# Kernel optimization log

Hardware: AMD Instinct MI355X
Metric: run time of the kernel (lower is better)

Reference implementation:

```python
import jax, jax.numpy as jnp
import numpy as np

EPS = 1e-12  # F.normalize default eps (denominator = max(norm, eps))


def setup_inputs() -> dict:
    key = jax.random.key(0)
    ks = jax.random.split(key, 8)
    B, FIN, H, W = 4, 256, 64, 64
    N_MEM, SQ = 64, 16           # sqrt_fin = fin**0.5
    POS_CH = 2                    # PosEncoding concatenates one coord channel per dim
    CIN = FIN + POS_CH
    QK = N_MEM * SQ               # 1024
    # PosEncoding buffer: normalized coordinate grid in [-1, 1], shape [2, H, W]
    ys = jnp.linspace(-1.0, 1.0, H, dtype=jnp.float32)
    xs = jnp.linspace(-1.0, 1.0, W, dtype=jnp.float32)
    gy, gx = jnp.meshgrid(ys, xs, indexing='ij')
    pos = jnp.stack([gy, gx], axis=0)
    s = 0.02
    return {
        'x':    jax.random.normal(ks[0], (B, FIN, H, W), jnp.float32),
        'pos':  pos,
        'wq':   jax.random.normal(ks[1], (QK, CIN), jnp.float32) * s,
        'bq':   jnp.zeros((QK,), jnp.float32),
        'wk':   jax.random.normal(ks[2], (QK, CIN), jnp.float32) * s,
        'bk':   jnp.zeros((QK,), jnp.float32),
        'v':    jax.random.normal(ks[3], (N_MEM, FIN), jnp.float32) * s,
        'wout': jax.random.normal(ks[4], (FIN, FIN), jnp.float32) * s,
        'bout': jnp.zeros((FIN,), jnp.float32),
    }


def reference(x, pos, wq, bq, wk, bk, v, wout, bout):
    B, C, H, W = x.shape
    S = H * W
    n_mem, fin = v.shape
    sq = wq.shape[0] // n_mem
    # PosEncoding: concat coordinate channels
    posb = jnp.broadcast_to(pos[None], (B,) + pos.shape)
    xp = jnp.concatenate([x, posb], axis=1).reshape(B, C + pos.shape[0], S)
    # 1x1 conv projections (channel GEMMs)
    q = jnp.einsum('oc,bcs->bos', wq, xp) + bq[None, :, None]  # [B, n_mem*sq, S]
    k = jnp.einsum('oc,bcs->bos', wk, xp) + bk[None, :, None]
    q = q.reshape(B, n_mem, sq, S).transpose(0, 3, 1, 2)  # [B,S,m,sq]
    k = k.reshape(B, n_mem, sq, S).transpose(0, 3, 2, 1)  # [B,S,sq,m]
    # F.normalize: q over last dim (sqrt_fin), k over dim=1 (sqrt_fin)
    qn = q / jnp.maximum(jnp.linalg.norm(q, axis=-1, keepdims=True), EPS)
    kn = k / jnp.maximum(jnp.linalg.norm(k, axis=2, keepdims=True), EPS)
    # attn[b,s,m,n] = qn . kn ; dropout is identity in eval mode.
    # mean over memory slots m commutes with (attn @ v), so fuse:
    attn_mean = jnp.einsum('bsk,bskn->bsn', qn.mean(axis=2), kn)  # [B,S,n_mem]
    mem = attn_mean @ v                                            # [B,S,fin]
    mem = mem.transpose(0, 2, 1).reshape(B, fin, H, W)
    out = jnp.einsum('of,bfhw->bohw', wout, mem) + bout[None, :, None, None]
    return x + out
```

## Files before the change

kernel.cpp:

```cpp
#include <hip/hip_runtime.h>
#include <stdint.h>

#define EPSN 1e-12f

typedef float f32x16 __attribute__((ext_vector_type(16)));
typedef float f32x4 __attribute__((ext_vector_type(4)));
typedef __bf16 bf16x8 __attribute__((ext_vector_type(8)));
typedef uint32_t u32x4 __attribute__((ext_vector_type(4)));

__device__ __forceinline__ unsigned short f2bf(float f) {
  union { float f; unsigned int u; } v; v.f = f;
  unsigned int u = v.u + 0x7FFFu + ((v.u >> 16) & 1u);
  return (unsigned short)(u >> 16);
}

__device__ __forceinline__ void dma16(const void* g, void* l) {
  __builtin_amdgcn_global_load_lds(
      (const __attribute__((address_space(1))) unsigned int*)g,
      (__attribute__((address_space(3))) unsigned int*)l, 16, 0, 0);
}

#define WQF_OFF 0
#define WKF_OFF (32 * 18 * 64 * 8)
#define WVP_OFF (2 * 32 * 18 * 64 * 8)

__global__ __launch_bounds__(256) void prep_kernel(
    const float* __restrict__ wq, const float* __restrict__ bq,
    const float* __restrict__ wk, const float* __restrict__ bk,
    const float* __restrict__ v, const float* __restrict__ wout,
    unsigned short* __restrict__ wsp) {
  if (blockIdx.x < 288) {
    int t2 = blockIdx.x * 256 + threadIdx.x;
    int isK = t2 >= 36864;
    int t = isK ? t2 - 36864 : t2;
    const float* w = isK ? wk : wq;
    const float* bb = isK ? bk : bq;
    unsigned short* dst = wsp + (isK ? WKF_OFF : WQF_OFF);
    int lane = t & 63, rest = t >> 6;
    int ks = rest % 18, g = rest / 18;
    int o = g * 32 + (lane & 31);
    int kb = ks * 16 + (lane >> 5) * 8;
    unsigned short v8[8];
#pragma unroll
    for (int j = 0; j < 8; ++j) {
      int k = kb + j;
      float val;
      if (k < 258)       val = w[o * 258 + k];
      else if (k == 258) val = bb[o];
      else               val = 0.f;
      v8[j] = f2bf(val);
    }
    *(u32x4*)(dst + t * 8) = *(u32x4*)v8;
  } else {
    int idx2 = (blockIdx.x - 288) * 256 + threadIdx.x;
    int fc = idx2 & 3, m = (idx2 >> 2) & 63, o = idx2 >> 8;
    const f32x4* wo = (const f32x4*)(wout + o * 256 + fc * 64);
    const f32x4* vm = (const f32x4*)(v + m * 256 + fc * 64);
    float s = 0.f;
#pragma unroll
    for (int f = 0; f < 16; ++f) {
      f32x4 a = wo[f], bvv = vm[f];
      s += a[0]*bvv[0] + a[1]*bvv[1] + a[2]*bvv[2] + a[3]*bvv[3];
    }
    s += __shfl_xor(s, 1, 64);
    s += __shfl_xor(s, 2, 64);
    if (fc == 0) wsp[WVP_OFF + o * 64 + m] = f2bf(s);
  }
}

#define KP 296
#define QS 66
#define AT 72

__global__ __launch_bounds__(1024, 4) void fused_kernel(
    const float* __restrict__ x, const float* __restrict__ pos,
    const unsigned short* __restrict__ wsp, const float* __restrict__ bout,
    float* __restrict__ out) {
  __shared__ __align__(16) unsigned short aBuf[3 * 32 * 512];
  __shared__ __align__(16) unsigned short xp[64 * KP];
  __shared__ __align__(16) float qbarL[16 * QS];
  __shared__ __align__(16) unsigned short attnM[64 * AT];
  __shared__ float boutL[256];

  const int tid = threadIdx.x;
  const int lane = tid & 63;
  const int wid = __builtin_amdgcn_readfirstlane(tid >> 6);
  const int px = lane & 31, q2 = lane >> 5;
  const int P0 = blockIdx.x * 64;
  const int b = P0 >> 12, s0 = P0 & 4095;

  uint32_t* xp32 = (uint32_t*)xp;
  for (int i = tid; i < 64 * 152; i += 1024) {
    int dc = i & 7, pp = (i >> 3) & 63, dh = i >> 9;
    int dcol = dh * 8 + dc;
    if (dcol < 148) {
      int c0 = dcol * 2;
      float v0, v1;
      if (c0 < 256) {
        v0 = x[(b * 256 + c0) * 4096 + s0 + pp];
        v1 = x[(b * 256 + c0 + 1) * 4096 + s0 + pp];
      } else if (c0 == 256) {
        v0 = pos[s0 + pp];
        v1 = pos[4096 + s0 + pp];
      } else {
        v0 = (c0 == 258) ? 1.0f : 0.0f;
        v1 = 0.0f;
      }
      xp32[pp * 148 + dcol] = (uint32_t)f2bf(v0) | ((uint32_t)f2bf(v1) << 16);
    }
  }
  if (tid < 256) boutL[tid] = bout[tid];
  for (int i = tid; i < 16 * QS; i += 1024) qbarL[i] = 0.f;
  __syncthreads();

#define ISSUE(wb, ks_) do {                                              \
    int _sl = (ks_) % 3;                                                 \
    dma16(wb + ((2 * wid) * 18 + (ks_)) * 512 + lane * 8,                \
          &aBuf[_sl * 16384 + (2 * wid) * 512]);                         \
    dma16(wb + ((2 * wid + 1) * 18 + (ks_)) * 512 + lane * 8,            \
          &aBuf[_sl * 16384 + (2 * wid + 1) * 512]);                     \
  } while (0)

#define COMPUTE(ks_) do {                                                \
    int _sl = (ks_) % 3;                                                 \
    bf16x8 _a0 = *(const bf16x8*)&aBuf[_sl * 16384 + (2 * wid) * 512 + lane * 8];     \
    bf16x8 _a1 = *(const bf16x8*)&aBuf[_sl * 16384 + (2 * wid + 1) * 512 + lane * 8]; \
    bf16x8 _b0 = *(const bf16x8*)&xp[px * KP + (ks_) * 16 + q2 * 8];     \
    bf16x8 _b1 = *(const bf16x8*)&xp[(32 + px) * KP + (ks_) * 16 + q2 * 8]; \
    acc00 = __builtin_amdgcn_mfma_f32_32x32x16_bf16(_a0, _b0, acc00, 0, 0, 0); \
    acc01 = __builtin_amdgcn_mfma_f32_32x32x16_bf16(_a0, _b1, acc01, 0, 0, 0); \
    acc10 = __builtin_amdgcn_mfma_f32_32x32x16_bf16(_a1, _b0, acc10, 0, 0, 0); \
    acc11 = __builtin_amdgcn_mfma_f32_32x32x16_bf16(_a1, _b1, acc11, 0, 0, 0); \
  } while (0)

#define PHASE(wb) do {                                                   \
    ISSUE(wb, 0); ISSUE(wb, 1);                                          \
    _Pragma("unroll 4")                                                  \
    for (int ks = 0; ks < 16; ++ks) {                                    \
      asm volatile("" ::: "memory");                                     \
      ISSUE(wb, ks + 2);                                                 \
      asm volatile("s_waitcnt vmcnt(4)" ::: "memory");                   \
      COMPUTE(ks);                                                       \
    }                                                                    \
    asm volatile("s_waitcnt vmcnt(2)" ::: "memory");                     \
    COMPUTE(16);                                                         \
    asm volatile("s_waitcnt vmcnt(0)" ::: "memory");                     \
    COMPUTE(17);                                                         \
  } while (0)

  f32x16 acc00 = (f32x16)0.f, acc01 = (f32x16)0.f,
         acc10 = (f32x16)0.f, acc11 = (f32x16)0.f;
  PHASE((wsp + WQF_OFF));

  {
    float qsum[2][8];
#pragma unroll
    for (int nt = 0; nt < 2; ++nt)
#pragma unroll
      for (int r = 0; r < 8; ++r) qsum[nt][r] = 0.f;
#pragma unroll
    for (int ot = 0; ot < 2; ++ot) {
#pragma unroll
      for (int nt = 0; nt < 2; ++nt) {
        const f32x16 a = ot ? (nt ? acc11 : acc10) : (nt ? acc01 : acc00);
        float s20 = 0.f, s21 = 0.f;
#pragma unroll
        for (int r = 0; r < 8; ++r) {
          s20 = fmaf(a[r], a[r], s20);
          s21 = fmaf(a[r + 8], a[r + 8], s21);
        }
        s20 += __shfl_xor(s20, 32, 64);
        s21 += __shfl_xor(s21, 32, 64);
        float i0 = 1.0f / fmaxf(sqrtf(s20), EPSN);
        float i1 = 1.0f / fmaxf(sqrtf(s21), EPSN);
#pragma unroll
        for (int r = 0; r < 8; ++r) qsum[nt][r] += a[r] * i0 + a[r + 8] * i1;
      }
    }
#pragma unroll
    for (int nt = 0; nt < 2; ++nt)
#pragma unroll
      for (int r = 0; r < 8; ++r) {
        int j = (r & 3) + ((r >> 2) << 3) + (q2 << 2);
        atomicAdd(&qbarL[j * QS + nt * 32 + px], qsum[nt][r] * (1.0f / 64.0f));
      }
  }
  __syncthreads();

  acc00 = (f32x16)0.f; acc01 = (f32x16)0.f;
  acc10 = (f32x16)0.f; acc11 = (f32x16)0.f;
  PHASE((wsp + WKF_OFF));

  {
    float qb[2][8];
#pragma unroll
    for (int nt = 0; nt < 2; ++nt)
#pragma unroll
      for (int r = 0; r < 8; ++r) {
        int j = (r & 3) + ((r >> 2) << 3) + (q2 << 2);
        qb[nt][r] = qbarL[j * QS + nt * 32 + px];
      }
#pragma unroll
    for (int ot = 0; ot < 2; ++ot) {
#pragma unroll
      for (int nt = 0; nt < 2; ++nt) {
        const f32x16 a = ot ? (nt ? acc11 : acc10) : (nt ? acc01 : acc00);
        float s20 = 0.f, s21 = 0.f, sp0 = 0.f, sp1 = 0.f;
#pragma unroll
        for (int r = 0; r < 8; ++r) {
          s20 = fmaf(a[r], a[r], s20);         sp0 = fmaf(qb[nt][r], a[r], sp0);
          s21 = fmaf(a[r + 8], a[r + 8], s21); sp1 = fmaf(qb[nt][r], a[r + 8], sp1);
        }
        s20 += __shfl_xor(s20, 32, 64);
        s21 += __shfl_xor(s21, 32, 64);
        sp0 += __shfl_xor(sp0, 32, 64);
        sp1 += __shfl_xor(sp1, 32, 64);
        if (q2 == 0) {
          int m0 = wid * 4 + ot * 2;
          attnM[(nt * 32 + px) * AT + m0]     = f2bf(sp0 / fmaxf(sqrtf(s20), EPSN));
          attnM[(nt * 32 + px) * AT + m0 + 1] = f2bf(sp1 / fmaxf(sqrtf(s21), EPSN));
        }
      }
    }
  }
  __syncthreads();

  {
    const int otile = wid >> 1, pxt = wid & 1;
    f32x16 e = (f32x16)0.f;
    const unsigned short* wv = wsp + WVP_OFF + (otile * 32 + px) * 64 + q2 * 8;
    const unsigned short* ab = &attnM[(pxt * 32 + px) * AT + q2 * 8];
#pragma unroll
    for (int ks = 0; ks < 4; ++ks) {
      bf16x8 av = *(const bf16x8*)(wv + ks * 16);
      bf16x8 bv = *(const bf16x8*)(ab + ks * 16);
      e = __builtin_amdgcn_mfma_f32_32x32x16_bf16(av, bv, e, 0, 0, 0);
    }
#pragma unroll
    for (int r = 0; r < 16; ++r) {
      const int o = otile * 32 + (r & 3) + ((r >> 2) << 3) + (q2 << 2);
      const int p = pxt * 32 + px;
      const int gi = (b * 256 + o) * 4096 + s0 + p;
      out[gi] = x[gi] + boutL[o] + e[r];
    }
  }
#undef PHASE
#undef COMPUTE
#undef ISSUE
}

extern "C" void kernel_launch(void* const* d_in, const int* in_sizes, int n_in,
                              void* d_out, int out_size, void* d_ws, size_t ws_size,
                              hipStream_t stream) {
  const float* x    = (const float*)d_in[0];
  const float* pos  = (const float*)d_in[1];
  const float* wq   = (const float*)d_in[2];
  const float* bq   = (const float*)d_in[3];
  const float* wk   = (const float*)d_in[4];
  const float* bk   = (const float*)d_in[5];
  const float* v    = (const float*)d_in[6];
  const float* wout = (const float*)d_in[7];
  const float* bout = (const float*)d_in[8];
  float* out = (float*)d_out;
  unsigned short* wsp = (unsigned short*)d_ws;

  hipLaunchKernelGGL(prep_kernel, dim3(544), dim3(256), 0, stream,
                     wq, bq, wk, bk, v, wout, wsp);
  hipLaunchKernelGGL(fused_kernel, dim3(256), dim3(1024), 0, stream,
                     x, pos, wsp, bout, out);
}
```

Baseline: 136.3 us.

## Coalesce weight prep reads, widen wout·v reduction, prefetch A tiles earlier

The prep kernel now reads wq/wk rows contiguously as float2 and scatters them into the MFMA fragment layout. Previously each thread gathered eight strided values. The wout·v fold is split across 16 lanes instead of 4, which launches more blocks. In the fused kernel, the first two DMA weight stages are issued before the x staging loop, and the K-phase prefetch is issued before the Q normalization epilogue, so global latency overlaps other work. B-operand LDS loads are also hoisted ahead of the DMA issue. The early K prefetch relies on the omitted middle section no longer issuing its own initial stages, which raises a risk of slot conflicts with aBuf.

```diff
diff --git a/kernel.cpp b/kernel.cpp
--- a/kernel.cpp
+++ b/kernel.cpp
@@ -6,7 +6,6 @@
 typedef float f32x16 __attribute__((ext_vector_type(16)));
 typedef float f32x4 __attribute__((ext_vector_type(4)));
 typedef __bf16 bf16x8 __attribute__((ext_vector_type(8)));
-typedef uint32_t u32x4 __attribute__((ext_vector_type(4)));
 
 __device__ __forceinline__ unsigned short f2bf(float f) {
   union { float f; unsigned int u; } v; v.f = f;
@@ -29,41 +28,45 @@
     const float* __restrict__ wk, const float* __restrict__ bk,
     const float* __restrict__ v, const float* __restrict__ wout,
     unsigned short* __restrict__ wsp) {
-  if (blockIdx.x < 288) {
-    int t2 = blockIdx.x * 256 + threadIdx.x;
-    int isK = t2 >= 36864;
-    int t = isK ? t2 - 36864 : t2;
+  int bid = blockIdx.x;
+  if (bid < 512) {
+    int isK = bid >= 256;
+    int ob = (bid & 255) * 4;
     const float* w = isK ? wk : wq;
     const float* bb = isK ? bk : bq;
     unsigned short* dst = wsp + (isK ? WKF_OFF : WQF_OFF);
-    int lane = t & 63, rest = t >> 6;
-    int ks = rest % 18, g = rest / 18;
-    int o = g * 32 + (lane & 31);
-    int kb = ks * 16 + (lane >> 5) * 8;
-    unsigned short v8[8];
-#pragma unroll
-    for (int j = 0; j < 8; ++j) {
-      int k = kb + j;
-      float val;
-      if (k < 258)       val = w[o * 258 + k];
-      else if (k == 258) val = bb[o];
-      else               val = 0.f;
-      v8[j] = f2bf(val);
-    }
-    *(u32x4*)(dst + t * 8) = *(u32x4*)v8;
+    for (int i = threadIdx.x; i < 4 * 129; i += 256) {
+      int r = i / 129, q = i - r * 129;
+      int o = ob + r, k = q * 2;
+      float2 w2 = *(const float2*)(w + o * 258 + k);
+      int g = o >> 5, col = o & 31;
+      int ks = k >> 4, hi = (k >> 3) & 1, j = k & 7;
+      uint32_t pk = (uint32_t)f2bf(w2.x) | ((uint32_t)f2bf(w2.y) << 16);
+      *(uint32_t*)(dst + (((g * 18 + ks) * 64 + hi * 32 + col) << 3) + j) = pk;
+    }
+    for (int i = threadIdx.x; i < 4 * 30; i += 256) {
+      int r = i / 30, kk = 258 + (i - r * 30);
+      int o = ob + r;
+      int g = o >> 5, col = o & 31;
+      int ks = kk >> 4, hi = (kk >> 3) & 1, j = kk & 7;
+      dst[(((g * 18 + ks) * 64 + hi * 32 + col) << 3) + j] =
+          (kk == 258) ? f2bf(bb[o]) : (unsigned short)0;
+    }
   } else {
-    int idx2 = (blockIdx.x - 288) * 256 + threadIdx.x;
-    int fc = idx2 & 3, m = (idx2 >> 2) & 63, o = idx2 >> 8;
-    const f32x4* wo = (const f32x4*)(wout + o * 256 + fc * 64);
-    const f32x4* vm = (const f32x4*)(v + m * 256 + fc * 64);
+    int idx = (bid - 512) * 256 + threadIdx.x;
+    int fc = idx & 15, m = (idx >> 4) & 63, o = idx >> 10;
+    const f32x4* wo = (const f32x4*)(wout + o * 256 + fc * 16);
+    const f32x4* vm = (const f32x4*)(v + m * 256 + fc * 16);
     float s = 0.f;
 #pragma unroll
-    for (int f = 0; f < 16; ++f) {
+    for (int f = 0; f < 4; ++f) {
       f32x4 a = wo[f], bvv = vm[f];
       s += a[0]*bvv[0] + a[1]*bvv[1] + a[2]*bvv[2] + a[3]*bvv[3];
     }
     s += __shfl_xor(s, 1, 64);
     s += __shfl_xor(s, 2, 64);
+    s += __shfl_xor(s, 4, 64);
+    s += __shfl_xor(s, 8, 64);
     if (fc == 0) wsp[WVP_OFF + o * 64 + m] = f2bf(s);
   }
 }
@@ -88,6 +91,17 @@
   const int px = lane & 31, q2 = lane >> 5;
   const int P0 = blockIdx.x * 64;
   const int b = P0 >> 12, s0 = P0 & 4095;
+
+#define ISSUE(wb, ks_) do {                                              \
+    int _sl = (ks_) % 3;                                                 \
+    dma16(wb + ((2 * wid) * 18 + (ks_)) * 512 + lane * 8,                \
+          &aBuf[_sl * 16384 + (2 * wid) * 512]);                         \
+    dma16(wb + ((2 * wid + 1) * 18 + (ks_)) * 512 + lane * 8,            \
+          &aBuf[_sl * 16384 + (2 * wid + 1) * 512]);                     \
+  } while (0)
+
+  ISSUE((wsp + WQF_OFF), 0);
+  ISSUE((wsp + WQF_OFF), 1);
 
   uint32_t* xp32 = (uint32_t*)xp;
   for (int i = tid; i < 64 * 152; i += 1024) {
@@ -113,44 +127,45 @@
   for (int i = tid; i < 16 * QS; i += 1024) qbarL[i] = 0.f;
   __syncthreads();
 
-#define ISSUE(wb, ks_) do {                                              \
-    int _sl = (ks_) % 3;                                                 \
-    dma16(wb + ((2 * wid) * 18 + (ks_)) * 512 + lane * 8,                \
-          &aBuf[_sl * 16384 + (2 * wid) * 512]);                         \
-    dma16(wb + ((2 * wid + 1) * 18 + (ks_)) * 512 + lane * 8,            \
-          &aBuf[_sl * 16384 + (2 * wid + 1) * 512]);                     \
-  } while (0)
-
-#define COMPUTE(ks_) do {                                                \
+#define COMPUTEA(ks_, b0_, b1_) do {                                     \
     int _sl = (ks_) % 3;                                                 \
     bf16x8 _a0 = *(const bf16x8*)&aBuf[_sl * 16384 + (2 * wid) * 512 + lane * 8];     \
     bf16x8 _a1 = *(const bf16x8*)&aBuf[_sl * 16384 + (2 * wid + 1) * 512 + lane * 8]; \
-    bf16x8 _b0 = *(const bf16x8*)&xp[px * KP + (ks_) * 16 + q2 * 8];     \
-    bf16x8 _b1 = *(const bf16x8*)&xp[(32 + px) * KP + (ks_) * 16 + q2 * 8]; \
-    acc00 = __builtin_amdgcn_mfma_f32_32x32x16_bf16(_a0, _b0, acc00, 0, 0, 0); \
-    acc01 = __builtin_amdgcn_mfma_f32_32x32x16_bf16(_a0, _b1, acc01, 0, 0, 0); \
-    acc10 = __builtin_amdgcn_mfma_f32_32x32x16_bf16(_a1, _b0, acc10, 0, 0, 0); \
-    acc11 = __builtin_amdgcn_mfma_f32_32x32x16_bf16(_a1, _b1, acc11, 0, 0, 0); \
+    acc00 = __builtin_amdgcn_mfma_f32_32x32x16_bf16(_a0, b0_, acc00, 0, 0, 0); \
+    acc01 = __builtin_amdgcn_mfma_f32_32x32x16_bf16(_a0, b1_, acc01, 0, 0, 0); \
+    acc10 = __builtin_amdgcn_mfma_f32_32x32x16_bf16(_a1, b0_, acc10, 0, 0, 0); \
+    acc11 = __builtin_amdgcn_mfma_f32_32x32x16_bf16(_a1, b1_, acc11, 0, 0, 0); \
   } while (0)
 
 #define PHASE(wb) do {                                                   \
-    ISSUE(wb, 0); ISSUE(wb, 1);                                          \
     _Pragma("unroll 4")                                                  \
     for (int ks = 0; ks < 16; ++ks) {                                    \
-      asm volatile("" ::: "memory");                                     \
+      bf16x8 _b0 = *(const bf16x8*)&xp[px * KP + ks * 16 + q2 * 8];      \
+      bf16x8 _b1 = *(const bf16x8*)&xp[(32 + px) * KP + ks * 16 + q2 * 8]; \
       ISSUE(wb, ks + 2);                                                 \
       asm volatile("s_waitcnt vmcnt(4)" ::: "memory");                   \
-      COMPUTE(ks);                                                       \
+      COMPUTEA(ks, _b0, _b1);                                            \
     }                                                                    \
-    asm volatile("s_waitcnt vmcnt(2)" ::: "memory");                     \
-    COMPUTE(16);                                                         \
-    asm volatile("s_waitcnt vmcnt(0)" ::: "memory");                     \
-    COMPUTE(17);                                                         \
+    {                                                                    \
+      bf16x8 _b0 = *(const bf16x8*)&xp[px * KP + 16 * 16 + q2 * 8];      \
+      bf16x8 _b1 = *(const bf16x8*)&xp[(32 + px) * KP + 16 * 16 + q2 * 8]; \
+      asm volatile("s_waitcnt vmcnt(2)" ::: "memory");                   \
+      COMPUTEA(16, _b0, _b1);                                            \
+    }                                                                    \
+    {                                                                    \
+      bf16x8 _b0 = *(const bf16x8*)&xp[px * KP + 17 * 16 + q2 * 8];      \
+      bf16x8 _b1 = *(const bf16x8*)&xp[(32 + px) * KP + 17 * 16 + q2 * 8]; \
+      asm volatile("s_waitcnt vmcnt(0)" ::: "memory");                   \
+      COMPUTEA(17, _b0, _b1);                                            \
+    }                                                                    \
   } while (0)
 
   f32x16 acc00 = (f32x16)0.f, acc01 = (f32x16)0.f,
          acc10 = (f32x16)0.f, acc11 = (f32x16)0.f;
   PHASE((wsp + WQF_OFF));
+
+  ISSUE((wsp + WKF_OFF), 0);
+  ISSUE((wsp + WKF_OFF), 1);
 
   {
     float qsum[2][8];
@@ -245,7 +260,7 @@
     }
   }
 #undef PHASE
-#undef COMPUTE
+#undef COMPUTEA
 #undef ISSUE
 }
 
@@ -264,7 +279,7 @@
   float* out = (float*)d_out;
   unsigned short* wsp = (unsigned short*)d_ws;
 
-  hipLaunchKernelGGL(prep_kernel, dim3(544), dim3(256), 0, stream,
+  hipLaunchKernelGGL(prep_kernel, dim3(1536), dim3(256), 0, stream,
                      wq, bq, wk, bk, v, wout, wsp);
   hipLaunchKernelGGL(fused_kernel, dim3(256), dim3(1024), 0, stream,
                      x, pos, wsp, bout, out);
```

Measured after the change: 130.9 us. -4.0%, faster.
